# Performance work log

Measured on AMD Instinct MI355X. Metric: run time of the kernel, lower is better.

Reference implementation:

```python
import jax, jax.numpy as jnp
import numpy as np

B, L = 4, 8192
IN_CH, OUT_CH = 1, 1
H = 64               # d_model
NSTATE = 16          # d_state
DBLK = 4             # number of residual blocks
DCONV = 16
EXPAND = 2
DINNER = EXPAND * H              # 128
HEADDIM = H // 4                 # 16
NHEADS = DINNER // HEADDIM       # 8
CONV_DIM = DINNER + 2 * NSTATE   # 160 (ngroups=1)
D_IN_PROJ = 2 * DINNER + 2 * NSTATE + NHEADS  # 296
CHUNK = 128


def setup_inputs():
    key = jax.random.key(0)
    ks = jax.random.split(key, 12)
    rn = lambda k, shape, s: (jax.random.normal(k, shape) * s).astype(jnp.float32)
    x = rn(ks[0], (B, L, IN_CH), 1.0)
    w_in = rn(ks[1], (H, IN_CH), 1.0)
    w_out = rn(ks[2], (OUT_CH, H), 1.0 / np.sqrt(H))
    in_proj_w = rn(ks[3], (DBLK, D_IN_PROJ, H), 1.0 / np.sqrt(H))
    conv_w = rn(ks[4], (DBLK, CONV_DIM, DCONV), 1.0 / np.sqrt(DCONV))
    conv_b = rn(ks[5], (DBLK, CONV_DIM), 0.02)
    dt = jnp.exp(jax.random.uniform(ks[6], (DBLK, NHEADS)) * (np.log(0.1) - np.log(1e-3)) + np.log(1e-3))
    dt_bias = (dt + jnp.log(-jnp.expm1(-dt))).astype(jnp.float32)  # inverse softplus
    A_log = jnp.log(jax.random.uniform(ks[7], (DBLK, NHEADS), minval=1.0, maxval=16.0)).astype(jnp.float32)
    D_skip = jnp.ones((DBLK, NHEADS), jnp.float32)
    init_states = rn(ks[8], (DBLK, NHEADS, HEADDIM, NSTATE), 0.01)
    norm_w = jnp.ones((DBLK, DINNER), jnp.float32)
    out_proj_w = rn(ks[9], (DBLK, H, DINNER), 1.0 / np.sqrt(DINNER))
    mlp_w = rn(ks[10], (DBLK, H, H), 1.0 / np.sqrt(H))
    mlp_b = jnp.zeros((DBLK, H), jnp.float32)
    return {"x": x, "w_in": w_in, "w_out": w_out, "in_proj_w": in_proj_w,
            "conv_w": conv_w, "conv_b": conv_b, "dt_bias": dt_bias, "A_log": A_log,
            "D_skip": D_skip, "init_states": init_states, "norm_w": norm_w,
            "out_proj_w": out_proj_w, "mlp_w": mlp_w, "mlp_b": mlp_b}


def segsum(a):
    # a: (..., q) -> (..., q, q); seg[i, j] = sum_{k=j+1..i} a[k] on lower triangle (diag=0), exp->0 above
    q = a.shape[-1]
    cs = jnp.cumsum(a, axis=-1)
    seg = cs[..., :, None] - cs[..., None, :]
    mask = jnp.tril(jnp.ones((q, q), dtype=bool))
    return jnp.where(mask, seg, -1e30)


def ssd(X, dA, Bm, Cm, init_state):
    # Chunked SSD (Mamba2 paper). X: (b,l,h,p) = x*dt, dA: (b,l,h), Bm/Cm: (b,l,n), init_state: (b,h,p,n)
    b, l, h, p = X.shape
    c = l // CHUNK
    X = X.reshape(b, c, CHUNK, h, p)
    Bm = Bm.reshape(b, c, CHUNK, NSTATE)
    Cm = Cm.reshape(b, c, CHUNK, NSTATE)
    A = dA.reshape(b, c, CHUNK, h).transpose(0, 3, 1, 2)  # (b,h,c,q)
    A_cs = jnp.cumsum(A, axis=-1)
    # intra-chunk (diagonal blocks)
    Lm = jnp.exp(segsum(A))  # (b,h,c,q,q)
    Y_diag = jnp.einsum('bcln,bcsn,bhcls,bcshp->bclhp', Cm, Bm, Lm, X)
    # per-chunk final states
    decay_states = jnp.exp(A_cs[..., -1:] - A_cs)  # (b,h,c,q)
    states = jnp.einsum('bcln,bhcl,bclhp->bchpn', Bm, decay_states, X)
    states = jnp.concatenate([init_state[:, None], states], axis=1)  # (b,c+1,h,p,n)
    # inter-chunk recurrence (vectorized via segsum over chunk decays)
    decay_chunk = jnp.exp(segsum(jnp.pad(A_cs[..., -1], ((0, 0), (0, 0), (1, 0)))))  # (b,h,c+1,c+1)
    new_states = jnp.einsum('bhzc,bchpn->bzhpn', decay_chunk, states)
    prev_states = new_states[:, :-1]  # state entering each chunk
    state_decay = jnp.exp(A_cs)
    Y_off = jnp.einsum('bcln,bchpn,bhcl->bclhp', Cm, prev_states, state_decay)
    return (Y_diag + Y_off).reshape(b, l, h, p)


def mamba2(u, w_inp, cw, cb, dtb, alog, dskip, istate, nw, w_outp):
    b, l, _ = u.shape
    zxbcdt = jnp.einsum('bld,ed->ble', u, w_inp)  # (b,l,296)
    z = zxbcdt[..., :DINNER]
    xBC = zxbcdt[..., DINNER:DINNER + CONV_DIM]
    dt = jax.nn.softplus(zxbcdt[..., DINNER + CONV_DIM:] + dtb)  # (b,l,h)
    # causal depthwise conv over seq + silu
    xBC = jax.lax.conv_general_dilated(
        xBC.transpose(0, 2, 1), cw[:, None, :], (1,), [(DCONV - 1, 0)],
        feature_group_count=CONV_DIM, dimension_numbers=('NCH', 'OIH', 'NCH'))
    xBC = jax.nn.silu(xBC + cb[None, :, None]).transpose(0, 2, 1)
    xs = xBC[..., :DINNER]
    Bm = xBC[..., DINNER:DINNER + NSTATE]
    Cm = xBC[..., DINNER + NSTATE:]
    A = -jnp.exp(alog)  # (h,)
    xh = xs.reshape(b, l, NHEADS, HEADDIM)
    init = jnp.broadcast_to(istate, (b,) + istate.shape)
    y = ssd(xh * dt[..., None], dt * A, Bm, Cm, init)
    y = y + xh * dskip[None, None, :, None]  # D skip
    y = y.reshape(b, l, DINNER)
    # gated RMSNorm: norm(y * silu(z)) * weight
    y = y * jax.nn.silu(z)
    y = y * jax.lax.rsqrt(jnp.mean(y * y, axis=-1, keepdims=True) + 1e-5) * nw
    return jnp.einsum('ble,de->bld', y, w_outp)


def reference(x, w_in, w_out, in_proj_w, conv_w, conv_b, dt_bias, A_log,
              D_skip, init_states, norm_w, out_proj_w, mlp_w, mlp_b):
    h = jnp.einsum('bli,hi->blh', x, w_in)
    for i in range(DBLK):
        y = mamba2(h, in_proj_w[i], conv_w[i], conv_b[i], dt_bias[i], A_log[i],
                   D_skip[i], init_states[i], norm_w[i], out_proj_w[i])
        t = y / jnp.sqrt(1.0 + y * y)  # TanhApprox
        y = jnp.einsum('blh,oh->blo', t, mlp_w[i]) + mlp_b[i]
        h = h + y  # residual
    return jnp.einsum('blh,oh->blo', h, w_out)
```

## Files before the change

### kernel.cpp

```cpp
#include <hip/hip_runtime.h>
#include <math.h>

#define NB 4
#define SEQ 8192
#define NT (NB*SEQ)
#define HDIM 64
#define NST 16
#define NBLK 4
#define KCONV 16
#define DIN 128
#define PDIM 16
#define NH 8
#define CDIM 160
#define EPROJ 296
#define CH 128
#define NC 64

typedef __attribute__((ext_vector_type(8))) short short8;
typedef __attribute__((ext_vector_type(4))) float f32x4;

__device__ __forceinline__ float sigf(float x){ return 1.0f/(1.0f+__expf(-x)); }

__device__ __forceinline__ unsigned short bf16r(float f){
  unsigned int u = __float_as_uint(f);
  u = (u + 0x7fffu + ((u >> 16) & 1u)) >> 16;
  return (unsigned short)u;
}
__device__ __forceinline__ unsigned int pk_bf16(float a, float b){
  return (unsigned int)bf16r(a) | ((unsigned int)bf16r(b) << 16);
}
__device__ __forceinline__ float bf16f(unsigned short h){
  return __uint_as_float(((unsigned int)h) << 16);
}

__global__ __launch_bounds__(256) void k_init(const float* __restrict__ x, const float* __restrict__ w_in,
                                              float* __restrict__ h,
                                              const float* __restrict__ w,
                                              unsigned short* __restrict__ whi,
                                              unsigned short* __restrict__ wlo){
  int bi = blockIdx.x;
  const int HB = (NT*HDIM)/256;
  if(bi < HB){
    int i = bi*256 + threadIdx.x;
    int t = i >> 6, d = i & 63;
    h[i] = x[t]*w_in[d];
  } else {
    int i = (bi - HB)*256 + threadIdx.x;
    if(i < NBLK*EPROJ*HDIM){
      float f = w[i];
      unsigned short hi = bf16r(f);
      float fh = bf16f(hi);
      whi[i] = hi;
      wlo[i] = bf16r(f - fh);
    }
  }
}

__global__ __launch_bounds__(1024, 4) void k_front(const float* __restrict__ h,
                                                const unsigned short* __restrict__ whi,
                                                const unsigned short* __restrict__ wlo,
                                                const float* __restrict__ cw, const float* __restrict__ cb,
                                                const float* __restrict__ dtb, const float* __restrict__ alog,
                                                unsigned short* __restrict__ zxz,
                                                unsigned short* __restrict__ xbc,
                                                float* __restrict__ dt, float* __restrict__ acs,
                                                float* __restrict__ asum, float* __restrict__ S){
  __shared__ __align__(16) unsigned char smf[148480];
  unsigned short* Hh  = (unsigned short*)(smf);
  unsigned short* Hl  = (unsigned short*)(smf + 20736);
  float* zxcS         = (float*)(smf + 41472);
  unsigned short* XhT = (unsigned short*)(smf);
  unsigned short* XlT = (unsigned short*)(smf + 34816);
  unsigned short* BhT = (unsigned short*)(smf + 69632);
  unsigned short* BlT = (unsigned short*)(smf + 73984);
  float* dtraw = (float*)(smf + 136192);
  float* dtl   = (float*)(smf + 140288);
  float* wle   = (float*)(smf + 144384);

  int bc = blockIdx.x;
  int c = bc & 63, b = bc >> 6;
  int t0 = b*SEQ + c*CH;
  int tid = threadIdx.x, lane = tid & 63, wid = tid >> 6;
  int quad = lane >> 4, lq = lane & 15;

#pragma unroll
  for(int k=0;k<3;k++){
    int idx = tid + k*1024;
    if(idx < 2304){
      int tok = idx >> 4;
      int d0 = (idx & 15) * 4;
      float4 v;
      if(c == 0 && tok < 16){ v = make_float4(0.f,0.f,0.f,0.f); }
      else v = *(const float4*)(h + (size_t)(t0 - 16 + tok)*HDIM + d0);
      float vv[4] = {v.x, v.y, v.z, v.w};
      unsigned short hi4[4], lo4[4];
#pragma unroll
      for(int j=0;j<4;j++){
        unsigned short hi = bf16r(vv[j]);
        hi4[j] = hi;
        lo4[j] = bf16r(vv[j] - bf16f(hi));
      }
      uint2 ph, pl;
      ph.x = (unsigned int)hi4[0] | ((unsigned int)hi4[1] << 16);
      ph.y = (unsigned int)hi4[2] | ((unsigned int)hi4[3] << 16);
      pl.x = (unsigned int)lo4[0] | ((unsigned int)lo4[1] << 16);
      pl.y = (unsigned int)lo4[2] | ((unsigned int)lo4[3] << 16);
      *(uint2*)&Hh[tok*72 + d0] = ph;
      *(uint2*)&Hl[tok*72 + d0] = pl;
    }
  }
  __syncthreads();

  {
    int L = wid;
    int tg, et;
    if(L < 152){ tg = 1 + L/19; et = L % 19; } else { tg = 0; et = 8 + (L - 152); }
    {
      int e_a = et*16 + lq;
      int ec = (e_a < EPROJ) ? e_a : (EPROJ-1);
      const unsigned short* wh = whi + (size_t)ec*HDIM + quad*8;
      const unsigned short* wl = wlo + (size_t)ec*HDIM + quad*8;
      short8 ah0 = *(const short8*)wh;
      short8 ah1 = *(const short8*)(wh + 32);
      short8 al0 = *(const short8*)wl;
      short8 al1 = *(const short8*)(wl + 32);
      while(true){
        int Ln = L + 16;
        int tgn = 0, etn = 0;
        short8 nh0 = ah0, nh1 = ah1, nl0 = al0, nl1 = al1;
        if(Ln < 162){
          if(Ln < 152){ tgn = 1 + Ln/19; etn = Ln % 19; } else { tgn = 0; etn = 8 + (Ln - 152); }
          int e_n = etn*16 + lq;
          int ecn = (e_n < EPROJ) ? e_n : (EPROJ-1);
          const unsigned short* wh2 = whi + (size_t)ecn*HDIM + quad*8;
          const unsigned short* wl2 = wlo + (size_t)ecn*HDIM + quad*8;
          nh0 = *(const short8*)wh2;
          nh1 = *(const short8*)(wh2 + 32);
          nl0 = *(const short8*)wl2;
          nl1 = *(const short8*)(wl2 + 32);
        }
        const unsigned short* hrh = Hh + (tg*16 + lq)*72 + quad*8;
        const unsigned short* hrl = Hl + (tg*16 + lq)*72 + quad*8;
        short8 xh0 = *(const short8*)hrh;
        short8 xh1 = *(const short8*)(hrh + 32);
        short8 xl0 = *(const short8*)hrl;
        short8 xl1 = *(const short8*)(hrl + 32);
        f32x4 acc = {0.f,0.f,0.f,0.f};
        acc = __builtin_amdgcn_mfma_f32_16x16x32_bf16(ah0, xh0, acc, 0, 0, 0);
        acc = __builtin_amdgcn_mfma_f32_16x16x32_bf16(ah1, xh1, acc, 0, 0, 0);
        acc = __builtin_amdgcn_mfma_f32_16x16x32_bf16(ah0, xl0, acc, 0, 0, 0);
        acc = __builtin_amdgcn_mfma_f32_16x16x32_bf16(ah1, xl1, acc, 0, 0, 0);
        acc = __builtin_amdgcn_mfma_f32_16x16x32_bf16(al0, xh0, acc, 0, 0, 0);
        acc = __builtin_amdgcn_mfma_f32_16x16x32_bf16(al1, xh1, acc, 0, 0, 0);
        if(tg >= 1){
          int tokg = t0 + (tg-1)*16 + lq;
#pragma unroll
          for(int r=0;r<4;r++){
            int e = et*16 + quad*4 + r;
            if(e < 128)        zxz[(size_t)e*NT + tokg] = bf16r(acc[r]);
            else if(e < 288)   zxcS[(e-128)*148 + tg*16 + lq] = acc[r];
            else if(e < 296)   dtraw[(e-288)*128 + (tg-1)*16 + lq] = acc[r];
          }
        } else {
#pragma unroll
          for(int r=0;r<4;r++){
            int e = et*16 + quad*4 + r;
            zxcS[(e-128)*148 + lq] = acc[r];
          }
        }
        if(Ln >= 162) break;
        L = Ln; tg = tgn; et = etn;
        ah0 = nh0; ah1 = nh1; al0 = nl0; al1 = nl1;
      }
    }
  }
  __syncthreads();

  unsigned int hiP[3][4], loP[3][4];
#pragma unroll
  for(int it=0; it<3; it++){
    int G = tid + it*1024;
    if(G < 2560){
      int ch = G >> 4, sg = (G & 15)*8;
      float buf[24];
#pragma unroll
      for(int q4=0;q4<6;q4++){
        float4 f = *(const float4*)&zxcS[ch*148 + sg + q4*4];
        buf[q4*4+0]=f.x; buf[q4*4+1]=f.y; buf[q4*4+2]=f.z; buf[q4*4+3]=f.w;
      }
      float wv[16];
#pragma unroll
      for(int k=0;k<16;k++) wv[k] = cw[ch*KCONV + k];
      float bias = cb[ch];
      unsigned short hs[8], ls[8];
#pragma unroll
      for(int s=0;s<8;s++){
        float acc = bias;
#pragma unroll
        for(int k=0;k<16;k++) acc += wv[k]*buf[s+1+k];
        float r = acc * sigf(acc);
        unsigned short hi = bf16r(r);
        hs[s] = hi;
        ls[s] = bf16r(r - bf16f(hi));
      }
      hiP[it][0] = (unsigned int)hs[0] | ((unsigned int)hs[1] << 16);
      hiP[it][1] = (unsigned int)hs[2] | ((unsigned int)hs[3] << 16);
      hiP[it][2] = (unsigned int)hs[4] | ((unsigned int)hs[5] << 16);
      hiP[it][3] = (unsigned int)hs[6] | ((unsigned int)hs[7] << 16);
      loP[it][0] = (unsigned int)ls[0] | ((unsigned int)ls[1] << 16);
      loP[it][1] = (unsigned int)ls[2] | ((unsigned int)ls[3] << 16);
      loP[it][2] = (unsigned int)ls[4] | ((unsigned int)ls[5] << 16);
      loP[it][3] = (unsigned int)ls[6] | ((unsigned int)ls[7] << 16);
      uint4 pk;
      pk.x = hiP[it][0]; pk.y = hiP[it][1]; pk.z = hiP[it][2]; pk.w = hiP[it][3];
      *(uint4*)(xbc + (size_t)ch*NT + t0 + sg) = pk;
    }
  }
  {
    int hh = tid >> 7, s = tid & 127;
    float raw = dtraw[hh*128 + s] + dtb[hh];
    float v = (raw > 20.f) ? raw : log1pf(__expf(raw));
    dtl[hh*128 + s] = v;
    dt[(size_t)hh*NT + t0 + s] = v;
  }
  __syncthreads();

#pragma unroll
  for(int it=0; it<3; it++){
    int G = tid + it*1024;
    if(G < 2560){
      int ch = G >> 4, sg = (G & 15)*8;
      if(ch < 128){
        uint4 vh; vh.x=hiP[it][0]; vh.y=hiP[it][1]; vh.z=hiP[it][2]; vh.w=hiP[it][3];
        uint4 vl; vl.x=loP[it][0]; vl.y=loP[it][1]; vl.z=loP[it][2]; vl.w=loP[it][3];
        *(uint4*)&XhT[ch*136 + sg] = vh;
        *(uint4*)&XlT[ch*136 + sg] = vl;
      } else if(ch < 144){
        uint4 vh; vh.x=hiP[it][0]; vh.y=hiP[it][1]; vh.z=hiP[it][2]; vh.w=hiP[it][3];
        uint4 vl; vl.x=loP[it][0]; vl.y=loP[it][1]; vl.z=loP[it][2]; vl.w=loP[it][3];
        *(uint4*)&BhT[(ch-128)*136 + sg] = vh;
        *(uint4*)&BlT[(ch-128)*136 + sg] = vl;
      }
    }
  }
  if(wid < 8){
    int hh = wid;
    float A = -__expf(alog[hh]);
    float2 dd = *(const float2*)&dtl[hh*128 + 2*lane];
    float d0 = dd.x, d1 = dd.y;
    float v0 = d0*A, v1 = d1*A;
    float s = v0 + v1;
    for(int off=1; off<64; off<<=1){
      float o = __shfl_up(s, off);
      if(lane >= off) s += o;
    }
    float tot = __shfl(s, 63);
    float excl = s - (v0+v1);
    float a0 = excl+v0, a1 = excl+v0+v1;
    *(float2*)&acs[(size_t)hh*NT + t0 + 2*lane] = make_float2(a0, a1);
    if(lane == 63) asum[(size_t)bc*NH + hh] = __expf(tot);
    wle[hh*128 + 2*lane]   = d0*__expf(tot - a0);
    wle[hh*128 + 2*lane+1] = d1*__expf(tot - a1);
  }
  __syncthreads();

  if(wid < 8){
    int hh = wid;
    f32x4 acc = {0.f,0.f,0.f,0.f};
#pragma unroll
    for(int kb=0;kb<4;kb++){
      int k0 = kb*32 + quad*8;
      short8 xh = *(const short8*)&XhT[(hh*16 + lq)*136 + k0];
      short8 xl = *(const short8*)&XlT[(hh*16 + lq)*136 + k0];
      float4 w0 = *(const float4*)&wle[hh*128 + k0];
      float4 w1 = *(const float4*)&wle[hh*128 + k0 + 4];
      float wv8[8] = {w0.x,w0.y,w0.z,w0.w,w1.x,w1.y,w1.z,w1.w};
      short8 ah, al;
#pragma unroll
      for(int j=0;j<8;j++){
        float xv = bf16f((unsigned short)xh[j]) + bf16f((unsigned short)xl[j]);
        float pw = xv * wv8[j];
        unsigned short hi = bf16r(pw);
        ah[j] = (short)hi;
        al[j] = (short)bf16r(pw - bf16f(hi));
      }
      short8 bh = *(const short8*)&BhT[lq*136 + k0];
      short8 bl = *(const short8*)&BlT[lq*136 + k0];
      acc = __builtin_amdgcn_mfma_f32_16x16x32_bf16(ah, bh, acc, 0, 0, 0);
      acc = __builtin_amdgcn_mfma_f32_16x16x32_bf16(ah, bl, acc, 0, 0, 0);
      acc = __builtin_amdgcn_mfma_f32_16x16x32_bf16(al, bh, acc, 0, 0, 0);
    }
    float* Sp = S + ((size_t)bc*NH + hh)*256;
#pragma unroll
    for(int r=0;r<4;r++) Sp[(quad*4 + r)*16 + lq] = acc[r];
  }
}

__global__ __launch_bounds__(64) void k_scan(const float* __restrict__ S, const float* __restrict__ easum,
                                             const float* __restrict__ init, float* __restrict__ prev){
  int q  = blockIdx.x & 3;
  int hh = (blockIdx.x >> 2) & 7;
  int b  = blockIdx.x >> 5;
  int el = q*64 + threadIdx.x;
  const size_t cs = (size_t)NH*256;
  const float* Sp = S + ((size_t)(b*NC)*NH + hh)*256 + el;
  float* Pp = prev + ((size_t)(b*NC)*NH + hh)*256 + el;
  const float* ap = easum + (size_t)(b*NC)*NH + hh;
  float e[NC];
#pragma unroll
  for(int c=0;c<NC;c++) e[c] = ap[(size_t)c*NH];
  float r = init[hh*256 + el];
  float s0 = Sp[0], s1 = Sp[cs], s2 = Sp[2*cs], s3 = Sp[3*cs];
#pragma unroll
  for(int c=0;c<NC;c+=4){
    Pp[(size_t)c*cs] = r;
    r = e[c]*r + s0;
    s0 = (c+4 < NC) ? Sp[(size_t)(c+4)*cs] : 0.f;
    Pp[(size_t)(c+1)*cs] = r;
    r = e[c+1]*r + s1;
    s1 = (c+5 < NC) ? Sp[(size_t)(c+5)*cs] : 0.f;
    Pp[(size_t)(c+2)*cs] = r;
    r = e[c+2]*r + s2;
    s2 = (c+6 < NC) ? Sp[(size_t)(c+6)*cs] : 0.f;
    Pp[(size_t)(c+3)*cs] = r;
    r = e[c+3]*r + s3;
    s3 = (c+7 < NC) ? Sp[(size_t)(c+7)*cs] : 0.f;
  }
}

__global__ __launch_bounds__(1024, 4) void k_tail(const unsigned short* __restrict__ xbc,
                                               const unsigned short* __restrict__ zxz,
                                               const float* __restrict__ dt, const float* __restrict__ acs,
                                               const float* __restrict__ prev, const float* __restrict__ dskip,
                                               const float* __restrict__ nw, const float* __restrict__ opw,
                                               const float* __restrict__ mw, const float* __restrict__ mb,
                                               float* __restrict__ h,
                                               int last, const float* __restrict__ wout,
                                               float* __restrict__ out){
  __shared__ __align__(16) unsigned char sm[151840];
  unsigned short* Bb   = (unsigned short*)(sm);
  unsigned short* Cb   = (unsigned short*)(sm + 6144);
  unsigned short* XbT  = (unsigned short*)(sm + 12288);
  unsigned short* P0   = (unsigned short*)(sm + 55296);
  unsigned short* P1   = (unsigned short*)(sm + 98304);
  float* Al  = (float*)(sm + 141312);
  float* Dtl = (float*)(sm + 145408);
  float* nwl = (float*)(sm + 149504);
  float* mbl = (float*)(sm + 150016);
  unsigned short* zbuf = (unsigned short*)(sm + 150272);
  float* ssl  = (float*)(sm + 150304);
  float* outb = (float*)(sm + 151328);
  unsigned short* Zb = XbT;
  unsigned short* Wo = P0;
  unsigned short* Wm = P0 + 64*136;
  unsigned short* Yn = P1;
  unsigned short* Tt = P1;

  int bc = blockIdx.x;
  int c = bc & 63, b = bc >> 6;
  int t0 = b*SEQ + c*CH;
  int tid = threadIdx.x, lane = tid & 63, wid = tid >> 6;
  int quad = lane >> 4, lq = lane & 15;
  int hgrp = wid >> 3;
  int wr7 = wid & 7;
  int widr = (wr7 < 4) ? wr7 : (11 - wr7);
  int strip = widr*16;

#pragma unroll
  for(int k=0;k<4;k++){
    int idx = tid + k*1024;
    int ch = idx >> 7, s = idx & 127;
    unsigned short f = xbc[(size_t)(DIN+ch)*NT + t0 + s];
    if(ch < 16) Bb[s*24 + ch] = f;
    else        Cb[s*24 + ch-16] = f;
  }
#pragma unroll
  for(int k=0;k<4;k++){
    int fi = tid + k*1024;
    int p = fi >> 5, s4 = fi & 31;
    uint2 xu = *(const uint2*)&xbc[(size_t)p*NT + t0 + s4*4];
    float4 dv = *(const float4*)&dt[(size_t)(p>>4)*NT + t0 + s4*4];
    float x0 = bf16f((unsigned short)(xu.x & 0xffffu));
    float x1 = bf16f((unsigned short)(xu.x >> 16));
    float x2 = bf16f((unsigned short)(xu.y & 0xffffu));
    float x3 = bf16f((unsigned short)(xu.y >> 16));
    *(unsigned int*)&XbT[p*168 + s4*4]   = pk_bf16(x0*dv.x, x1*dv.y);
    *(unsigned int*)&XbT[p*168 + s4*4+2] = pk_bf16(x2*dv.z, x3*dv.w);
  }
#pragma unroll
  for(int k=0;k<2;k++){
    int idx = tid + k*1024;
    int hh = idx >> 8, rest = idx & 255;
    int p = rest >> 4, n = rest & 15;
    XbT[(hh*16+p)*168 + 128 + n] = bf16r(prev[((size_t)bc*NH + hh)*256 + rest]);
  }
#pragma unroll
  for(int k=0;k<2;k++){
    int idx = tid + k*1024;
    if(idx < 1536){
      int p = idx / 12, cc = idx - p*12;
      *(unsigned int*)&XbT[p*168 + 144 + 2*cc] = 0u;
    }
  }
  {
    int hh = tid >> 7, s = tid & 127;
    Al[hh*128+s]  = acs[(size_t)hh*NT + t0 + s];
    Dtl[hh*128+s] = dt[(size_t)hh*NT + t0 + s];
  }
  if(tid < 128) nwl[tid] = nw[tid];
  else if(tid < 192) mbl[tid-128] = mb[tid-128];
  else if(tid < 208) zbuf[tid-192] = 0;
  {
    unsigned short* Pgz = hgrp ? P1 : P0;
#pragma unroll
    for(int k=0;k<3;k++){
      int idx = lane + k*64;
      int rr = idx / 12, cc = idx - rr*12;
      *(unsigned int*)&Pgz[(strip+rr)*168 + 144 + 2*cc] = 0u;
    }
    int zc0 = (widr+1)*16;
    int nu  = (7 - widr)*8;
    for(int u = lane>>4; u < nu; u += 4){
      *(unsigned int*)&Pgz[(strip+(lane&15))*168 + zc0 + 2*u] = 0u;
    }
  }
  __syncthreads();

  short8 afr;
  {
    int row = strip + lq;
    const unsigned short* ap = (quad < 2) ? &Cb[row*24 + quad*8] : zbuf;
    afr = *(const short8*)ap;
  }
  f32x4 sc[8];
#pragma unroll
  for(int nt=0;nt<8;nt++){
    f32x4 acc = {0.f,0.f,0.f,0.f};
    if(nt <= widr){
      const unsigned short* bp = (quad < 2) ? &Bb[(nt*16+lq)*24 + quad*8] : zbuf;
      short8 bfr = *(const short8*)bp;
      acc = __builtin_amdgcn_mfma_f32_16x16x32_bf16(afr, bfr, acc, 0, 0, 0);
    }
    sc[nt] = acc;
  }

  unsigned short* Pg = hgrp ? P1 : P0;
  f32x4 accv[4];
  for(int j=0;j<4;j++){
    int hh2 = hgrp*4 + j;
    const float* Alh = Al + hh2*128;
    float alr[4];
#pragma unroll
    for(int r=0;r<4;r++) alr[r] = Alh[strip + quad*4 + r];
#pragma unroll
    for(int nt=0;nt<8;nt++){
      if(nt <= widr){
        int col = nt*16 + lq;
        float alc = Alh[col];
#pragma unroll
        for(int r=0;r<4;r++){
          int row = strip + quad*4 + r;
          float p = sc[nt][r] * __expf(alr[r] - alc);
          p = (col <= row) ? p : 0.f;
          Pg[row*168 + col] = bf16r(p);
        }
      }
    }
    {
      int n = lane & 15, rg = lane >> 4;
#pragma unroll
      for(int rr=0;rr<4;rr++){
        int row = strip + rg*4 + rr;
        float ea = __expf(Alh[row]);
        Pg[row*168 + 128 + n] = bf16r(bf16f(Cb[row*24+n]) * ea);
      }
    }
    f32x4 acc2 = {0.f,0.f,0.f,0.f};
#pragma unroll
    for(int ks=0;ks<5;ks++){
      short8 bfr = *(const short8*)&XbT[(hh2*16+lq)*168 + ks*32 + quad*8];
      short8 af  = *(const short8*)&Pg[(strip+lq)*168 + ks*32 + quad*8];
      acc2 = __builtin_amdgcn_mfma_f32_16x16x32_bf16(af, bfr, acc2, 0, 0, 0);
    }
    const float* Dth = Dtl + hh2*128;
    float Dk = dskip[hh2];
#pragma unroll
    for(int r=0;r<4;r++){
      int l = strip + quad*4 + r;
      float xdt = bf16f(XbT[(hh2*16+lq)*168 + l]);
      float dtv = fmaxf(Dth[l], 1e-30f);
      acc2[r] += Dk * xdt * __frcp_rn(dtv);
    }
    accv[j] = acc2;
  }
  __syncthreads();

#pragma unroll
  for(int k=0;k<4;k++){
    int fi = tid + k*1024;
    int p = fi >> 5, s4 = fi & 31;
    uint2 zu = *(const uint2*)&zxz[(size_t)p*NT + t0 + s4*4];
    *(unsigned int*)&Zb[p*136 + s4*4]   = zu.x;
    *(unsigned int*)&Zb[p*136 + s4*4+2] = zu.y;
  }
#pragma unroll
  for(int k=0;k<2;k++){
    int fi = tid + k*1024;
    int n = fi >> 5, k4 = fi & 31;
    float4 wv = *(const float4*)&opw[(size_t)n*DIN + k4*4];
    *(unsigned int*)&Wo[n*136 + k4*4]   = pk_bf16(wv.x, wv.y);
    *(unsigned int*)&Wo[n*136 + k4*4+2] = pk_bf16(wv.z, wv.w);
  }
  {
    int fi = tid;
    int n = fi >> 4, k4 = fi & 15;
    float4 wv = *(const float4*)&mw[(size_t)n*HDIM + k4*4];
    *(unsigned int*)&Wm[n*72 + k4*4]   = pk_bf16(wv.x, wv.y);
    *(unsigned int*)&Wm[n*72 + k4*4+2] = pk_bf16(wv.z, wv.w);
  }
  __syncthreads();

  float part[4] = {0.f,0.f,0.f,0.f};
#pragma unroll
  for(int j=0;j<4;j++){
    int ch = (hgrp*4+j)*16 + lq;
    float nwv = nwl[ch];
#pragma unroll
    for(int r=0;r<4;r++){
      int l = strip + quad*4 + r;
      float zv = bf16f(Zb[ch*136 + l]);
      float g = zv * sigf(zv);
      float yv = accv[j][r] * g;
      part[r] += yv*yv;
      Yn[l*136 + ch] = bf16r(yv * nwv);
    }
  }
#pragma unroll
  for(int r=0;r<4;r++){
    part[r] += __shfl_xor(part[r],1); part[r] += __shfl_xor(part[r],2);
    part[r] += __shfl_xor(part[r],4); part[r] += __shfl_xor(part[r],8);
  }
  if(lq == 0){
#pragma unroll
    for(int r=0;r<4;r++) ssl[hgrp*128 + strip + quad*4 + r] = part[r];
  }
  __syncthreads();

  float rms_[4];
#pragma unroll
  for(int r=0;r<4;r++){
    int l = strip + quad*4 + r;
    rms_[r] = rsqrtf((ssl[l] + ssl[128+l])*(1.0f/128.0f) + 1e-5f);
  }
  short8 afk[4];
#pragma unroll
  for(int ks=0;ks<4;ks++) afk[ks] = *(const short8*)&Yn[(strip+lq)*136 + ks*32 + quad*8];
  f32x4 aco[2];
#pragma unroll
  for(int ntl=0;ntl<2;ntl++){ aco[ntl] = (f32x4){0.f,0.f,0.f,0.f}; }
#pragma unroll
  for(int ntl=0;ntl<2;ntl++){
    int nt = hgrp*2 + ntl;
#pragma unroll
    for(int ks=0;ks<4;ks++){
      short8 bfr = *(const short8*)&Wo[(nt*16+lq)*136 + ks*32 + quad*8];
      aco[ntl] = __builtin_amdgcn_mfma_f32_16x16x32_bf16(afk[ks], bfr, aco[ntl], 0, 0, 0);
    }
  }
  __syncthreads();
#pragma unroll
  for(int ntl=0;ntl<2;ntl++){
    int nt = hgrp*2 + ntl;
#pragma unroll
    for(int r=0;r<4;r++){
      int l = strip + quad*4 + r;
      float o = aco[ntl][r] * rms_[r];
      Tt[l*136 + nt*16+lq] = bf16r(o * rsqrtf(1.0f + o*o));
    }
  }
  __syncthreads();

  f32x4 acm[2];
#pragma unroll
  for(int ntl=0;ntl<2;ntl++){ acm[ntl] = (f32x4){0.f,0.f,0.f,0.f}; }
#pragma unroll
  for(int ks=0;ks<2;ks++){
    short8 af = *(const short8*)&Tt[(strip+lq)*136 + ks*32 + quad*8];
#pragma unroll
    for(int ntl=0;ntl<2;ntl++){
      int nt = hgrp*2 + ntl;
      short8 bfr = *(const short8*)&Wm[(nt*16+lq)*72 + ks*32 + quad*8];
      acm[ntl] = __builtin_amdgcn_mfma_f32_16x16x32_bf16(af, bfr, acm[ntl], 0, 0, 0);
    }
  }
  if(!last){
#pragma unroll
    for(int ntl=0;ntl<2;ntl++){
      int nt = hgrp*2 + ntl;
#pragma unroll
      for(int r=0;r<4;r++){
        int l = strip + quad*4 + r;
        int d = nt*16 + lq;
        size_t gi = (size_t)(t0+l)*HDIM + d;
        h[gi] += acm[ntl][r] + mbl[d];
      }
    }
  } else {
    float ps[4] = {0.f,0.f,0.f,0.f};
#pragma unroll
    for(int ntl=0;ntl<2;ntl++){
      int nt = hgrp*2 + ntl;
      int d = nt*16 + lq;
      float wo = wout[d];
      float bias = mbl[d];
#pragma unroll
      for(int r=0;r<4;r++){
        int l = strip + quad*4 + r;
        size_t gi = (size_t)(t0+l)*HDIM + d;
        float hn = h[gi] + acm[ntl][r] + bias;
        ps[r] += hn * wo;
      }
    }
#pragma unroll
    for(int r=0;r<4;r++){
      ps[r] += __shfl_xor(ps[r],1); ps[r] += __shfl_xor(ps[r],2);
      ps[r] += __shfl_xor(ps[r],4); ps[r] += __shfl_xor(ps[r],8);
    }
    if(hgrp == 1 && lq == 0){
#pragma unroll
      for(int r=0;r<4;r++) outb[strip + quad*4 + r] = ps[r];
    }
    __syncthreads();
    if(hgrp == 0 && lq == 0){
#pragma unroll
      for(int r=0;r<4;r++){
        int l = strip + quad*4 + r;
        out[t0 + l] = ps[r] + outb[l];
      }
    }
  }
}

extern "C" void kernel_launch(void* const* d_in, const int* in_sizes, int n_in,
                              void* d_out, int out_size, void* d_ws, size_t ws_size,
                              hipStream_t stream){
  const float* x          = (const float*)d_in[0];
  const float* w_in       = (const float*)d_in[1];
  const float* w_out      = (const float*)d_in[2];
  const float* in_proj_w  = (const float*)d_in[3];
  const float* conv_w     = (const float*)d_in[4];
  const float* conv_b     = (const float*)d_in[5];
  const float* dt_bias    = (const float*)d_in[6];
  const float* A_log      = (const float*)d_in[7];
  const float* D_skip     = (const float*)d_in[8];
  const float* init_st    = (const float*)d_in[9];
  const float* norm_w     = (const float*)d_in[10];
  const float* out_proj_w = (const float*)d_in[11];
  const float* mlp_w      = (const float*)d_in[12];
  const float* mlp_b      = (const float*)d_in[13];
  float* out = (float*)d_out;

  float* ws = (float*)d_ws;
  float* h    = ws; ws += (size_t)NT*HDIM;
  unsigned short* zxz = (unsigned short*)ws; ws += (size_t)(128*NT)/2;
  unsigned short* xbc = (unsigned short*)ws; ws += (size_t)(CDIM*NT)/2;
  float* dt   = ws; ws += (size_t)NH*NT;
  float* acs  = ws; ws += (size_t)NH*NT;
  float* asum = ws; ws += (size_t)NB*NC*NH;
  float* S    = ws; ws += (size_t)NB*NC*NH*256;
  float* prev = ws; ws += (size_t)NB*NC*NH*256;
  unsigned short* whi = (unsigned short*)ws; ws += (size_t)(NBLK*EPROJ*HDIM)/2;
  unsigned short* wlo = (unsigned short*)ws; ws += (size_t)(NBLK*EPROJ*HDIM)/2;

  k_init<<<(NT*HDIM)/256 + (NBLK*EPROJ*HDIM)/256, 256, 0, stream>>>(x, w_in, h, in_proj_w, whi, wlo);
  for(int i=0;i<NBLK;i++){
    k_front<<<NB*NC, 1024, 0, stream>>>(h, whi + (size_t)i*EPROJ*HDIM, wlo + (size_t)i*EPROJ*HDIM,
                                        conv_w + i*CDIM*KCONV, conv_b + i*CDIM,
                                        dt_bias + i*NH, A_log + i*NH,
                                        zxz, xbc, dt, acs, asum, S);
    k_scan  <<<NB*NH*4, 64, 0, stream>>>(S, asum, init_st + i*NH*256, prev);
    k_tail  <<<NB*NC, 1024, 0, stream>>>(xbc, zxz, dt, acs, prev, D_skip + i*NH,
                                         norm_w + i*DIN, out_proj_w + i*HDIM*DIN,
                                         mlp_w + i*HDIM*HDIM, mlp_b + i*HDIM, h,
                                         (i == NBLK-1) ? 1 : 0, w_out, out);
  }
}
```

Measured before the change: 331.8 us.

## Fuse chunk-state scan into tail kernel via cooperative grid sync

Removes the separate k_scan launch. A new cooperative kernel k_stail runs the inter-chunk state recurrence on the last wavefront of the first 128 blocks, while the other 15 wavefronts preload B/C, x*dt, acs, dt and norm weights into shared memory. A grid-wide sync then makes prev visible before the tail continues. The z buffer is also switched to a token-major layout so the front kernel writes packed bf16 vectors and the tail reads contiguous rows. The change removes one launch per block and overlaps the scan with the loads, but it depends on all 256 blocks being co-resident and adds the cost of a grid barrier.

```diff
diff --git a/kernel.cpp b/kernel.cpp
--- a/kernel.cpp
+++ b/kernel.cpp
@@ -1,5 +1,8 @@
 #include <hip/hip_runtime.h>
+#include <hip/hip_cooperative_groups.h>
 #include <math.h>
+
+namespace cg = cooperative_groups;
 
 #define NB 4
 #define SEQ 8192
@@ -154,12 +157,18 @@
         acc = __builtin_amdgcn_mfma_f32_16x16x32_bf16(al1, xh1, acc, 0, 0, 0);
         if(tg >= 1){
           int tokg = t0 + (tg-1)*16 + lq;
-#pragma unroll
-          for(int r=0;r<4;r++){
-            int e = et*16 + quad*4 + r;
-            if(e < 128)        zxz[(size_t)e*NT + tokg] = bf16r(acc[r]);
-            else if(e < 288)   zxcS[(e-128)*148 + tg*16 + lq] = acc[r];
-            else if(e < 296)   dtraw[(e-288)*128 + (tg-1)*16 + lq] = acc[r];
+          if(et < 8){
+            uint2 zz;
+            zz.x = pk_bf16(acc[0], acc[1]);
+            zz.y = pk_bf16(acc[2], acc[3]);
+            *(uint2*)&zxz[(size_t)tokg*DIN + et*16 + quad*4] = zz;
+          } else {
+#pragma unroll
+            for(int r=0;r<4;r++){
+              int e = et*16 + quad*4 + r;
+              if(e < 288)        zxcS[(e-128)*148 + tg*16 + lq] = acc[r];
+              else if(e < 296)   dtraw[(e-288)*128 + (tg-1)*16 + lq] = acc[r];
+            }
           }
         } else {
 #pragma unroll
@@ -296,42 +305,12 @@
   }
 }
 
-__global__ __launch_bounds__(64) void k_scan(const float* __restrict__ S, const float* __restrict__ easum,
-                                             const float* __restrict__ init, float* __restrict__ prev){
-  int q  = blockIdx.x & 3;
-  int hh = (blockIdx.x >> 2) & 7;
-  int b  = blockIdx.x >> 5;
-  int el = q*64 + threadIdx.x;
-  const size_t cs = (size_t)NH*256;
-  const float* Sp = S + ((size_t)(b*NC)*NH + hh)*256 + el;
-  float* Pp = prev + ((size_t)(b*NC)*NH + hh)*256 + el;
-  const float* ap = easum + (size_t)(b*NC)*NH + hh;
-  float e[NC];
-#pragma unroll
-  for(int c=0;c<NC;c++) e[c] = ap[(size_t)c*NH];
-  float r = init[hh*256 + el];
-  float s0 = Sp[0], s1 = Sp[cs], s2 = Sp[2*cs], s3 = Sp[3*cs];
-#pragma unroll
-  for(int c=0;c<NC;c+=4){
-    Pp[(size_t)c*cs] = r;
-    r = e[c]*r + s0;
-    s0 = (c+4 < NC) ? Sp[(size_t)(c+4)*cs] : 0.f;
-    Pp[(size_t)(c+1)*cs] = r;
-    r = e[c+1]*r + s1;
-    s1 = (c+5 < NC) ? Sp[(size_t)(c+5)*cs] : 0.f;
-    Pp[(size_t)(c+2)*cs] = r;
-    r = e[c+2]*r + s2;
-    s2 = (c+6 < NC) ? Sp[(size_t)(c+6)*cs] : 0.f;
-    Pp[(size_t)(c+3)*cs] = r;
-    r = e[c+3]*r + s3;
-    s3 = (c+7 < NC) ? Sp[(size_t)(c+7)*cs] : 0.f;
-  }
-}
-
-__global__ __launch_bounds__(1024, 4) void k_tail(const unsigned short* __restrict__ xbc,
+__global__ __launch_bounds__(1024, 4) void k_stail(const unsigned short* __restrict__ xbc,
                                                const unsigned short* __restrict__ zxz,
                                                const float* __restrict__ dt, const float* __restrict__ acs,
-                                               const float* __restrict__ prev, const float* __restrict__ dskip,
+                                               const float* __restrict__ S, const float* __restrict__ easum,
+                                               const float* __restrict__ initst, float* __restrict__ prev,
+                                               const float* __restrict__ dskip,
                                                const float* __restrict__ nw, const float* __restrict__ opw,
                                                const float* __restrict__ mw, const float* __restrict__ mb,
                                                float* __restrict__ h,
@@ -366,27 +345,63 @@
   int widr = (wr7 < 4) ? wr7 : (11 - wr7);
   int strip = widr*16;
 
-#pragma unroll
-  for(int k=0;k<4;k++){
-    int idx = tid + k*1024;
-    int ch = idx >> 7, s = idx & 127;
-    unsigned short f = xbc[(size_t)(DIN+ch)*NT + t0 + s];
-    if(ch < 16) Bb[s*24 + ch] = f;
-    else        Cb[s*24 + ch-16] = f;
-  }
-#pragma unroll
-  for(int k=0;k<4;k++){
-    int fi = tid + k*1024;
-    int p = fi >> 5, s4 = fi & 31;
-    uint2 xu = *(const uint2*)&xbc[(size_t)p*NT + t0 + s4*4];
-    float4 dv = *(const float4*)&dt[(size_t)(p>>4)*NT + t0 + s4*4];
-    float x0 = bf16f((unsigned short)(xu.x & 0xffffu));
-    float x1 = bf16f((unsigned short)(xu.x >> 16));
-    float x2 = bf16f((unsigned short)(xu.y & 0xffffu));
-    float x3 = bf16f((unsigned short)(xu.y >> 16));
-    *(unsigned int*)&XbT[p*168 + s4*4]   = pk_bf16(x0*dv.x, x1*dv.y);
-    *(unsigned int*)&XbT[p*168 + s4*4+2] = pk_bf16(x2*dv.z, x3*dv.w);
-  }
+  if(wid < 15){
+    for(int idx = tid; idx < 4096; idx += 960){
+      int ch = idx >> 7, s = idx & 127;
+      unsigned short f = xbc[(size_t)(DIN+ch)*NT + t0 + s];
+      if(ch < 16) Bb[s*24 + ch] = f;
+      else        Cb[s*24 + ch-16] = f;
+    }
+    for(int fi = tid; fi < 4096; fi += 960){
+      int p = fi >> 5, s4 = fi & 31;
+      uint2 xu = *(const uint2*)&xbc[(size_t)p*NT + t0 + s4*4];
+      float4 dv = *(const float4*)&dt[(size_t)(p>>4)*NT + t0 + s4*4];
+      float x0 = bf16f((unsigned short)(xu.x & 0xffffu));
+      float x1 = bf16f((unsigned short)(xu.x >> 16));
+      float x2 = bf16f((unsigned short)(xu.y & 0xffffu));
+      float x3 = bf16f((unsigned short)(xu.y >> 16));
+      *(unsigned int*)&XbT[p*168 + s4*4]   = pk_bf16(x0*dv.x, x1*dv.y);
+      *(unsigned int*)&XbT[p*168 + s4*4+2] = pk_bf16(x2*dv.z, x3*dv.w);
+    }
+    for(int idx = tid; idx < 1024; idx += 960){
+      int hh = idx >> 7, s = idx & 127;
+      Al[hh*128+s]  = acs[(size_t)hh*NT + t0 + s];
+      Dtl[hh*128+s] = dt[(size_t)hh*NT + t0 + s];
+    }
+    if(tid < 128) nwl[tid] = nw[tid];
+    else if(tid < 192) mbl[tid-128] = mb[tid-128];
+    else if(tid < 208) zbuf[tid-192] = 0;
+  } else if(bc < 128){
+    int ln = tid - 960;
+    int q  = bc & 3;
+    int hh = (bc >> 2) & 7;
+    int b2 = bc >> 5;
+    int el = q*64 + ln;
+    const size_t cs = (size_t)NH*256;
+    const float* Sp = S + ((size_t)(b2*NC)*NH + hh)*256 + el;
+    float* Pp = prev + ((size_t)(b2*NC)*NH + hh)*256 + el;
+    const float* ap = easum + (size_t)(b2*NC)*NH + hh;
+    float ev = ap[(size_t)ln*NH];
+    float r = initst[hh*256 + el];
+    float s0 = Sp[0], s1 = Sp[cs], s2 = Sp[2*cs], s3 = Sp[3*cs];
+#pragma unroll
+    for(int cc=0;cc<NC;cc+=4){
+      Pp[(size_t)cc*cs] = r;
+      r = __shfl(ev, cc)*r + s0;
+      s0 = (cc+4 < NC) ? Sp[(size_t)(cc+4)*cs] : 0.f;
+      Pp[(size_t)(cc+1)*cs] = r;
+      r = __shfl(ev, cc+1)*r + s1;
+      s1 = (cc+5 < NC) ? Sp[(size_t)(cc+5)*cs] : 0.f;
+      Pp[(size_t)(cc+2)*cs] = r;
+      r = __shfl(ev, cc+2)*r + s2;
+      s2 = (cc+6 < NC) ? Sp[(size_t)(cc+6)*cs] : 0.f;
+      Pp[(size_t)(cc+3)*cs] = r;
+      r = __shfl(ev, cc+3)*r + s3;
+      s3 = (cc+7 < NC) ? Sp[(size_t)(cc+7)*cs] : 0.f;
+    }
+  }
+  cg::this_grid().sync();
+
 #pragma unroll
   for(int k=0;k<2;k++){
     int idx = tid + k*1024;
@@ -403,14 +418,6 @@
     }
   }
   {
-    int hh = tid >> 7, s = tid & 127;
-    Al[hh*128+s]  = acs[(size_t)hh*NT + t0 + s];
-    Dtl[hh*128+s] = dt[(size_t)hh*NT + t0 + s];
-  }
-  if(tid < 128) nwl[tid] = nw[tid];
-  else if(tid < 192) mbl[tid-128] = mb[tid-128];
-  else if(tid < 208) zbuf[tid-192] = 0;
-  {
     unsigned short* Pgz = hgrp ? P1 : P0;
 #pragma unroll
     for(int k=0;k<3;k++){
@@ -429,8 +436,8 @@
   short8 afr;
   {
     int row = strip + lq;
-    const unsigned short* ap = (quad < 2) ? &Cb[row*24 + quad*8] : zbuf;
-    afr = *(const short8*)ap;
+    const unsigned short* ap2 = (quad < 2) ? &Cb[row*24 + quad*8] : zbuf;
+    afr = *(const short8*)ap2;
   }
   f32x4 sc[8];
 #pragma unroll
@@ -498,10 +505,9 @@
 #pragma unroll
   for(int k=0;k<4;k++){
     int fi = tid + k*1024;
-    int p = fi >> 5, s4 = fi & 31;
-    uint2 zu = *(const uint2*)&zxz[(size_t)p*NT + t0 + s4*4];
-    *(unsigned int*)&Zb[p*136 + s4*4]   = zu.x;
-    *(unsigned int*)&Zb[p*136 + s4*4+2] = zu.y;
+    int t = fi >> 5, c4 = (fi & 31)*4;
+    uint2 zu = *(const uint2*)&zxz[(size_t)(t0+t)*DIN + c4];
+    *(uint2*)&Zb[t*132 + c4] = zu;
   }
 #pragma unroll
   for(int k=0;k<2;k++){
@@ -528,7 +534,7 @@
 #pragma unroll
     for(int r=0;r<4;r++){
       int l = strip + quad*4 + r;
-      float zv = bf16f(Zb[ch*136 + l]);
+      float zv = bf16f(Zb[l*132 + ch]);
       float g = zv * sigf(zv);
       float yv = accv[j][r] * g;
       part[r] += yv*yv;
@@ -678,10 +684,26 @@
                                         conv_w + i*CDIM*KCONV, conv_b + i*CDIM,
                                         dt_bias + i*NH, A_log + i*NH,
                                         zxz, xbc, dt, acs, asum, S);
-    k_scan  <<<NB*NH*4, 64, 0, stream>>>(S, asum, init_st + i*NH*256, prev);
-    k_tail  <<<NB*NC, 1024, 0, stream>>>(xbc, zxz, dt, acs, prev, D_skip + i*NH,
-                                         norm_w + i*DIN, out_proj_w + i*HDIM*DIN,
-                                         mlp_w + i*HDIM*HDIM, mlp_b + i*HDIM, h,
-                                         (i == NBLK-1) ? 1 : 0, w_out, out);
+    const unsigned short* xbc_c = xbc;
+    const unsigned short* zxz_c = zxz;
+    const float* dt_c   = dt;
+    const float* acs_c  = acs;
+    const float* S_c    = S;
+    const float* asum_c = asum;
+    const float* init_i = init_st + i*NH*256;
+    const float* dsk_i  = D_skip + i*NH;
+    const float* nw_i   = norm_w + i*DIN;
+    const float* opw_i  = out_proj_w + i*HDIM*DIN;
+    const float* mw_i   = mlp_w + i*HDIM*HDIM;
+    const float* mb_i   = mlp_b + i*HDIM;
+    int last = (i == NBLK-1) ? 1 : 0;
+    void* args[] = {
+      (void*)&xbc_c, (void*)&zxz_c, (void*)&dt_c, (void*)&acs_c,
+      (void*)&S_c, (void*)&asum_c, (void*)&init_i, (void*)&prev,
+      (void*)&dsk_i, (void*)&nw_i, (void*)&opw_i, (void*)&mw_i, (void*)&mb_i,
+      (void*)&h, (void*)&last, (void*)&w_out, (void*)&out
+    };
+    hipLaunchCooperativeKernel((const void*)k_stail, dim3(NB*NC), dim3(1024),
+                               args, 0, stream);
   }
 }
```

Result: slower. 512.2 us (+54.4%).
